# Kernel tuning notes

Hardware: AMD Instinct MI355X
Metric: run time of the kernel (lower is better)

The kernel has to match this reference:

```python
import jax, jax.numpy as jnp
import numpy as np

N = 4096          # sequence length for both series
BIG = 1e30        # sentinel for invalid / out-of-band DP cells (fp32-safe)


def setup_inputs() -> dict:
    key = jax.random.key(0)
    k1, k2 = jax.random.split(key)
    return {
        "source": jax.random.normal(k1, (N,), dtype=jnp.float32),
        "target": jax.random.normal(k2, (N,), dtype=jnp.float32),
    }


def _shift(a):
    # a[i] -> a[i-1], shifting in BIG at i=0 (out-of-range DP cell)
    return jnp.concatenate([jnp.full((1,), BIG, a.dtype), a[:-1]])


def _dtw(x, y):
    """Exact DTW distance between 1-D series x, y (equal length n) with
    dist(a, b) = |a - b| (fastdtw's default 1-D metric).

    DP recurrence D[i, j] = c[i, j] + min(D[i-1, j], D[i, j-1], D[i-1, j-1])
    computed as an antidiagonal wavefront: diagonal k holds cells (i, k-i).
    Carry = (diag k-2, diag k-1), each a length-n vector indexed by i.
    """
    n = x.shape[0]
    i = jnp.arange(n)

    def step(carry, k):
        d2, d1 = carry            # D on diagonals k-2 and k-1
        j = k - i                 # column index for row i on diagonal k
        valid = (j >= 0) & (j < n)
        c = jnp.abs(x - y[jnp.clip(j, 0, n - 1)])  # local cost |x_i - y_j|
        # D[i, j-1] lives at d1[i]; D[i-1, j] at d1[i-1]; D[i-1, j-1] at d2[i-1]
        m = jnp.minimum(d1, jnp.minimum(_shift(d1), _shift(d2)))
        m = jnp.where((k == 0) & (i == 0), jnp.zeros_like(m), m)  # D[0,0] = c[0,0]
        d = jnp.where(valid, c + m, BIG)
        return (d1, d), None

    init = (jnp.full((n,), BIG, x.dtype), jnp.full((n,), BIG, x.dtype))
    (_, d_last), _ = jax.lax.scan(step, init, jnp.arange(2 * n - 1))
    return d_last[n - 1]  # D[n-1, n-1]


def reference(source, target):
    # Original module: fastdtw(source, target, radius=1) -> scalar distance.
    # We compute the exact DTW distance that fastdtw approximates.
    return _dtw(source, target)
```

## Files before the change

### kernel.cpp

```cpp
#include <hip/hip_runtime.h>

#define N     4096
#define TPB   512
#define KB    8
#define RSZ   32
#define NW    (TPB / 64)
#define BIG   1e30f
#define YIDXf(j) ((j) + (((j) >> 4) << 2))
#define NCHH   1024
#define STEPSH 1592

#define DPP_SHR1(res, oldv, srcv)                                         \
    res = __int_as_float(__builtin_amdgcn_update_dpp(                     \
        __float_as_int(oldv), __float_as_int(srcv), 0x138, 0xF, 0xF, false));


__global__ __launch_bounds__(TPB, 1)
void dtw_half_c2(const float* __restrict__ xg, const float* __restrict__ yg,
                 float* __restrict__ ws, int* __restrict__ cnt,
                 float* __restrict__ out) {
    __shared__ float  ylds[2048 + 2048 / 4 + 4];
    __shared__ float2 ring2[NW - 1][RSZ];
    __shared__ float  red[NW];

    const int t = threadIdx.x, lane = t & 63, w = t >> 6;
    const int b = blockIdx.x;

    for (int j = t; j < 2048; j += TPB)
        ylds[YIDXf(j)] = b ? yg[N - 1 - j] : yg[j];

    float x[8], carry[8];
    const int i0 = t * 8;
#pragma unroll
    for (int r = 0; r < 8; ++r) {
        x[r] = b ? xg[N - 1 - (i0 + r)] : xg[i0 + r];
        carry[r] = BIG;
    }

    float diagc = (t == 0) ? 0.0f : BIG;
    const int start = t + KB * w;
    const bool wring = (lane == 63) && (w < NW - 1);

    float bt0 = BIG, bt1 = BIG;
    float nb0 = BIG, nb1 = BIG;

    __syncthreads();
    float2 yv = *(const float2*)&ylds[0];

    for (int sb = 0; sb < STEPSH; sb += KB) {
        float2 nbring[KB];
        if (w > 0) {
            const int base = sb + 1 - 72 * w;
#pragma unroll
            for (int k = 0; k < KB; ++k)
                nbring[k] = ring2[w - 1][(base + k) & (RSZ - 1)];
        } else {
#pragma unroll
            for (int k = 0; k < KB; ++k)
                nbring[k] = make_float2(BIG, BIG);
        }

#pragma unroll
        for (int ss = 0; ss < KB; ++ss) {
            const int s = sb + ss;
            const int c = s - start;

            if ((unsigned)c < (unsigned)NCHH) {
#define DO_COL(YC, NB, DG, BT)                                            \
                { float up = (NB), dgv = (DG);                            \
                  _Pragma("unroll")                                       \
                  for (int r = 0; r < 8; ++r) {                           \
                      const float old = carry[r];                         \
                      const float v = fabsf(x[r] - (YC)) +                \
                                      fminf(up, fminf(old, dgv));         \
                      carry[r] = v; up = v; dgv = old;                    \
                  }                                                       \
                  (BT) = up; }
                DO_COL(yv.x, nb0, diagc, bt0)
                DO_COL(yv.y, nb1, nb0,   bt1)
#undef DO_COL
                diagc = nb1;
                if (wring)
                    ring2[w][c & (RSZ - 1)] = make_float2(bt0, bt1);
            }

            {
                const float2 oldv = nbring[ss];
                DPP_SHR1(nb0, oldv.x, bt0)
                DPP_SHR1(nb1, oldv.y, bt1)
                const unsigned cc = min((unsigned)(c + 1), (unsigned)(NCHH - 1));
                yv = *(const float2*)&ylds[YIDXf(2 * cc)];
            }
            asm volatile("" ::: "memory");
        }
        __syncthreads();
    }

    {
        float4* dst = (float4*)(ws + (size_t)b * 4096 + i0);
        dst[0] = make_float4(carry[0], carry[1], carry[2], carry[3]);
        dst[1] = make_float4(carry[4], carry[5], carry[6], carry[7]);
    }
    __syncthreads();

    if (t == 0) {
        __hip_atomic_fetch_add(cnt, 1, __ATOMIC_ACQ_REL, __HIP_MEMORY_SCOPE_AGENT);
        while (__hip_atomic_load(cnt, __ATOMIC_ACQUIRE,
                                 __HIP_MEMORY_SCOPE_AGENT) < 2) {}
    }
    __syncthreads();

    if (b == 1) {
        const float4 f0 = *(const float4*)&ws[i0];
        const float4 f1 = *(const float4*)&ws[i0 + 4];
        const float4 ba = *(const float4*)&ws[4096 + (4088 - i0)];
        const float4 bb = *(const float4*)&ws[4096 + (4092 - i0)];
        const float F[8]  = {f0.x, f0.y, f0.z, f0.w, f1.x, f1.y, f1.z, f1.w};
        const float B0[8] = {bb.w, bb.z, bb.y, bb.x, ba.w, ba.z, ba.y, ba.x};
        const float b1_7 = (i0 + 7 < N - 1) ? ws[4096 + (4087 - i0)] : BIG;
        const float B1[8] = {B0[1], B0[2], B0[3], B0[4], B0[5], B0[6], B0[7], b1_7};
        float m = BIG;
#pragma unroll
        for (int r = 0; r < 8; ++r)
            m = fminf(m, F[r] + fminf(B0[r], B1[r]));
#pragma unroll
        for (int o = 32; o >= 1; o >>= 1) m = fminf(m, __shfl_xor(m, o));
        if (lane == 0) red[w] = m;
        __syncthreads();
        if (t == 0) {
            float mm = red[0];
#pragma unroll
            for (int k = 1; k < NW; ++k) mm = fminf(mm, red[k]);
            out[0] = mm;
        }
    }
}

#define C    4
#define NCH  (N / C)
#define YIDX4(c) (((c) << 2) + (((c) >> 2) << 2))
__global__ __launch_bounds__(TPB, 1)
void dtw_diet(const float* __restrict__ xg, const float* __restrict__ yg,
              float* __restrict__ out) {
    __shared__ float  ylds[N + N / 4 + 4];
    __shared__ float4 bot4[2][TPB];
    __shared__ float4 ring4[NW - 1][RSZ];
    __shared__ float4 bigv;

    const int t = threadIdx.x, lane = t & 63, w = t >> 6;
    for (int j4 = t * 4; j4 < N; j4 += TPB * 4)
        *(float4*)&ylds[YIDX4(j4 >> 2)] = *(const float4*)&yg[j4];
    if (t == 0) bigv = make_float4(BIG, BIG, BIG, BIG);

    float x[8], carry[8];
    const int i0 = t * 8;
#pragma unroll
    for (int r = 0; r < 8; ++r) { x[r] = xg[i0 + r]; carry[r] = BIG; }
    float diagc = (t == 0) ? 0.0f : BIG;
    const int start = t + KB * w;
    const bool wring = (lane == 63) && (w < NW - 1);
    const int  tm1 = (t > 0) ? t - 1 : 0;
    __syncthreads();

    float4 nb4 = make_float4(BIG, BIG, BIG, BIG);
    float4 yv = *(const float4*)&ylds[0];

    for (int sb = 0; sb < 1592; sb += KB) {
        for (int ss = 0; ss < KB; ++ss) {
            const int s = sb + ss;
            const int c = s - start;
            if ((unsigned)c < (unsigned)NCH) {
                float bt0, bt1, bt2, bt3;
#define DO_COL(YC, NB, DG, BT)                                            \
                { float up = (NB), dgv = (DG);                            \
                  _Pragma("unroll")                                       \
                  for (int r = 0; r < 8; ++r) {                           \
                      const float old = carry[r];                         \
                      const float v = fabsf(x[r] - (YC)) +                \
                                      fminf(up, fminf(old, dgv));         \
                      carry[r] = v; up = v; dgv = old;                    \
                  }                                                       \
                  (BT) = up; }
                DO_COL(yv.x, nb4.x, diagc, bt0)
                DO_COL(yv.y, nb4.y, nb4.x, bt1)
                DO_COL(yv.z, nb4.z, nb4.y, bt2)
                DO_COL(yv.w, nb4.w, nb4.z, bt3)
#undef DO_COL
                diagc = nb4.w;
                float4* wp = wring ? &ring4[w][c & (RSZ - 1)]
                                   : &bot4[s & 1][t];
                *wp = make_float4(bt0, bt1, bt2, bt3);
            }
            {
                const int c1 = c + 1;
                const float4* rp;
                if (lane == 0)
                    rp = (w == 0) ? &bigv : &ring4[w - 1][c1 & (RSZ - 1)];
                else
                    rp = &bot4[s & 1][tm1];
                nb4 = *rp;
                const unsigned cc = min((unsigned)c1, (unsigned)(NCH - 1));
                yv = *(const float4*)&ylds[YIDX4(cc)];
            }
            asm volatile("" ::: "memory");
        }
        __syncthreads();
    }
    if (t == TPB - 1) out[0] = carry[7];
}

extern "C" void kernel_launch(void* const* d_in, const int* in_sizes, int n_in,
                              void* d_out, int out_size, void* d_ws, size_t ws_size,
                              hipStream_t stream) {
    const float* src = (const float*)d_in[0];
    const float* tgt = (const float*)d_in[1];
    float* out = (float*)d_out;

    const size_t req = 8192 * sizeof(float) + 64;
    if (ws_size >= req) {
        float* ws  = (float*)d_ws;
        int*   cnt = (int*)((char*)d_ws + 8192 * sizeof(float));
        hipMemsetAsync(cnt, 0, 64, stream);
        hipLaunchKernelGGL(dtw_half_c2, dim3(2), dim3(TPB), 0, stream,
                           src, tgt, ws, cnt, out);
    } else {
        hipLaunchKernelGGL(dtw_diet, dim3(1), dim3(TPB), 0, stream,
                           src, tgt, out);
    }
}
```

Before: 332.6 us.

## Use 256 threads with 16 rows each in split-half DTW wavefront

Each block now runs 256 threads, and each thread owns 16 DP rows instead of 8. This shortens the wavefront pipeline from 1592 to 1304 steps and halves the number of waves, which cuts ring and DPP handoff overhead. The y-value LDS load is also double-buffered one step ahead to hide LDS latency. In exchange, each thread runs a longer serial dependency chain per column and uses more registers. The merge step is rewritten to use scalar global loads.

After: 378.8 us. 1.14x slower.

```diff
diff --git a/kernel.cpp b/kernel.cpp
--- a/kernel.cpp
+++ b/kernel.cpp
@@ -1,53 +1,61 @@
 #include <hip/hip_runtime.h>
 
 #define N     4096
-#define TPB   512
 #define KB    8
 #define RSZ   32
-#define NW    (TPB / 64)
 #define BIG   1e30f
 #define YIDXf(j) ((j) + (((j) >> 4) << 2))
-#define NCHH   1024
-#define STEPSH 1592
 
 #define DPP_SHR1(res, oldv, srcv)                                         \
     res = __int_as_float(__builtin_amdgcn_update_dpp(                     \
         __float_as_int(oldv), __float_as_int(srcv), 0x138, 0xF, 0xF, false));
 
 
-__global__ __launch_bounds__(TPB, 1)
-void dtw_half_c2(const float* __restrict__ xg, const float* __restrict__ yg,
+#define TPB3   256
+#define RR3    16
+#define NCHH   1024
+#define STEPS3 1304
+
+__global__ __launch_bounds__(TPB3, 1)
+void dtw_half_v2(const float* __restrict__ xg, const float* __restrict__ yg,
                  float* __restrict__ ws, int* __restrict__ cnt,
                  float* __restrict__ out) {
     __shared__ float  ylds[2048 + 2048 / 4 + 4];
-    __shared__ float2 ring2[NW - 1][RSZ];
-    __shared__ float  red[NW];
+    __shared__ float2 ring2[3][RSZ];
+    __shared__ float  red[4];
 
     const int t = threadIdx.x, lane = t & 63, w = t >> 6;
     const int b = blockIdx.x;
 
-    for (int j = t; j < 2048; j += TPB)
+    for (int j = t; j < 2048; j += TPB3)
         ylds[YIDXf(j)] = b ? yg[N - 1 - j] : yg[j];
 
-    float x[8], carry[8];
-    const int i0 = t * 8;
-#pragma unroll
-    for (int r = 0; r < 8; ++r) {
+    float x[RR3], carry[RR3];
+    const int i0 = t * RR3;
+#pragma unroll
+    for (int r = 0; r < RR3; ++r) {
         x[r] = b ? xg[N - 1 - (i0 + r)] : xg[i0 + r];
         carry[r] = BIG;
     }
 
     float diagc = (t == 0) ? 0.0f : BIG;
     const int start = t + KB * w;
-    const bool wring = (lane == 63) && (w < NW - 1);
+    const bool wring = (lane == 63) && (w < 3);
 
     float bt0 = BIG, bt1 = BIG;
     float nb0 = BIG, nb1 = BIG;
 
     __syncthreads();
-    float2 yv = *(const float2*)&ylds[0];
-
-    for (int sb = 0; sb < STEPSH; sb += KB) {
+
+    float2 yv_cur, yv_nxt;
+    {
+        int c0 = 0 - start; c0 = c0 < 0 ? 0 : c0;
+        int c1 = 1 - start; c1 = c1 < 0 ? 0 : c1;
+        yv_cur = *(const float2*)&ylds[YIDXf(2 * c0)];
+        yv_nxt = *(const float2*)&ylds[YIDXf(2 * c1)];
+    }
+
+    for (int sb = 0; sb < STEPS3; sb += KB) {
         float2 nbring[KB];
         if (w > 0) {
             const int base = sb + 1 - 72 * w;
@@ -69,15 +77,15 @@
 #define DO_COL(YC, NB, DG, BT)                                            \
                 { float up = (NB), dgv = (DG);                            \
                   _Pragma("unroll")                                       \
-                  for (int r = 0; r < 8; ++r) {                           \
+                  for (int r = 0; r < RR3; ++r) {                         \
                       const float old = carry[r];                         \
                       const float v = fabsf(x[r] - (YC)) +                \
                                       fminf(up, fminf(old, dgv));         \
                       carry[r] = v; up = v; dgv = old;                    \
                   }                                                       \
                   (BT) = up; }
-                DO_COL(yv.x, nb0, diagc, bt0)
-                DO_COL(yv.y, nb1, nb0,   bt1)
+                DO_COL(yv_cur.x, nb0, diagc, bt0)
+                DO_COL(yv_cur.y, nb1, nb0,   bt1)
 #undef DO_COL
                 diagc = nb1;
                 if (wring)
@@ -88,8 +96,10 @@
                 const float2 oldv = nbring[ss];
                 DPP_SHR1(nb0, oldv.x, bt0)
                 DPP_SHR1(nb1, oldv.y, bt1)
-                const unsigned cc = min((unsigned)(c + 1), (unsigned)(NCHH - 1));
-                yv = *(const float2*)&ylds[YIDXf(2 * cc)];
+                yv_cur = yv_nxt;
+                int cn = c + 2;
+                cn = cn < 0 ? 0 : (cn > NCHH - 1 ? NCHH - 1 : cn);
+                yv_nxt = *(const float2*)&ylds[YIDXf(2 * cn)];
             }
             asm volatile("" ::: "memory");
         }
@@ -98,8 +108,10 @@
 
     {
         float4* dst = (float4*)(ws + (size_t)b * 4096 + i0);
-        dst[0] = make_float4(carry[0], carry[1], carry[2], carry[3]);
-        dst[1] = make_float4(carry[4], carry[5], carry[6], carry[7]);
+#pragma unroll
+        for (int q = 0; q < 4; ++q)
+            dst[q] = make_float4(carry[4 * q], carry[4 * q + 1],
+                                 carry[4 * q + 2], carry[4 * q + 3]);
     }
     __syncthreads();
 
@@ -111,33 +123,28 @@
     __syncthreads();
 
     if (b == 1) {
-        const float4 f0 = *(const float4*)&ws[i0];
-        const float4 f1 = *(const float4*)&ws[i0 + 4];
-        const float4 ba = *(const float4*)&ws[4096 + (4088 - i0)];
-        const float4 bb = *(const float4*)&ws[4096 + (4092 - i0)];
-        const float F[8]  = {f0.x, f0.y, f0.z, f0.w, f1.x, f1.y, f1.z, f1.w};
-        const float B0[8] = {bb.w, bb.z, bb.y, bb.x, ba.w, ba.z, ba.y, ba.x};
-        const float b1_7 = (i0 + 7 < N - 1) ? ws[4096 + (4087 - i0)] : BIG;
-        const float B1[8] = {B0[1], B0[2], B0[3], B0[4], B0[5], B0[6], B0[7], b1_7};
         float m = BIG;
 #pragma unroll
-        for (int r = 0; r < 8; ++r)
-            m = fminf(m, F[r] + fminf(B0[r], B1[r]));
+        for (int r = 0; r < RR3; ++r) {
+            const int i = i0 + r;
+            const float F  = ws[i];
+            const float B0 = ws[4096 + (N - 1 - i)];
+            const float B1 = (i < N - 1) ? ws[4096 + (N - 2 - i)] : BIG;
+            m = fminf(m, F + fminf(B0, B1));
+        }
 #pragma unroll
         for (int o = 32; o >= 1; o >>= 1) m = fminf(m, __shfl_xor(m, o));
         if (lane == 0) red[w] = m;
         __syncthreads();
-        if (t == 0) {
-            float mm = red[0];
-#pragma unroll
-            for (int k = 1; k < NW; ++k) mm = fminf(mm, red[k]);
-            out[0] = mm;
-        }
+        if (t == 0)
+            out[0] = fminf(fminf(red[0], red[1]), fminf(red[2], red[3]));
     }
 }
 
+#define TPB  512
 #define C    4
 #define NCH  (N / C)
+#define NW   (TPB / 64)
 #define YIDX4(c) (((c) << 2) + (((c) >> 2) << 2))
 __global__ __launch_bounds__(TPB, 1)
 void dtw_diet(const float* __restrict__ xg, const float* __restrict__ yg,
@@ -221,7 +228,7 @@
         float* ws  = (float*)d_ws;
         int*   cnt = (int*)((char*)d_ws + 8192 * sizeof(float));
         hipMemsetAsync(cnt, 0, 64, stream);
-        hipLaunchKernelGGL(dtw_half_c2, dim3(2), dim3(TPB), 0, stream,
+        hipLaunchKernelGGL(dtw_half_v2, dim3(2), dim3(TPB3), 0, stream,
                            src, tgt, ws, cnt, out);
     } else {
         hipLaunchKernelGGL(dtw_diet, dim3(1), dim3(TPB), 0, stream,
```
